# Optimization experiments

Hardware: AMD Instinct MI355X
Metric: run time of the kernel (lower is better)

The kernel has to match this reference:

```python
import jax, jax.numpy as jnp
import numpy as np

D_MODEL = 256
N_LEVELS = 4
N_HEADS = 8
N_POINTS = 4
OFF_DIM = 32
D_HEAD = D_MODEL // N_HEADS
SHAPES = [(64, 64), (32, 32), (16, 16), (8, 8)]  # (H_l, W_l)
LEN_IN = sum(h * w for h, w in SHAPES)  # 5440
N_BATCH = 4
LEN_Q = LEN_IN


def _offset_bias_init():
    # replicates _reset_parameters grid_init for sampling_offsets_bias
    thetas = np.arange(N_HEADS, dtype=np.float32) * (2.0 * np.pi / N_HEADS)
    grid = np.stack([np.cos(thetas), np.sin(thetas)], -1)
    grid = grid / np.abs(grid).max(-1, keepdims=True)
    grid = np.tile(grid[:, None, None, :], (1, N_LEVELS, N_POINTS, 1))
    grid = grid * np.arange(1, N_POINTS + 1, dtype=np.float32)[None, None, :, None]
    return jnp.asarray(grid, jnp.float32)  # (H, L, K, 2)


def setup_inputs() -> dict:
    key = jax.random.key(0)
    ks = jax.random.split(key, 12)
    s = 0.02
    return {
        "query": jax.random.normal(ks[0], (N_BATCH, LEN_Q, D_MODEL), jnp.float32),
        "reference_points": jax.random.uniform(ks[1], (N_BATCH, LEN_Q, N_LEVELS, 2), jnp.float32),
        "input_flatten": jax.random.normal(ks[2], (N_BATCH, LEN_IN, D_MODEL), jnp.float32),
        "input_spatial_shapes": jnp.asarray(SHAPES, jnp.int32),
        "offset_embeds_W": jax.random.normal(ks[3], (N_HEADS * N_LEVELS * N_POINTS * OFF_DIM, D_MODEL), jnp.float32) * s,
        "sampling_offsets_W": jax.random.normal(ks[4], (N_HEADS, N_LEVELS, N_POINTS, OFF_DIM, 2), jnp.float32) * s,
        "sampling_offsets_b": _offset_bias_init(),
        "attn_W": jax.random.normal(ks[5], (N_HEADS, N_LEVELS, N_POINTS, OFF_DIM, 1), jnp.float32) * s,
        "attn_b": jax.random.normal(ks[6], (N_HEADS, N_LEVELS, N_POINTS), jnp.float32) * s,
        "value_W": jax.random.normal(ks[7], (D_MODEL, D_MODEL), jnp.float32) * (1.0 / np.sqrt(D_MODEL)),
        "value_b": jnp.zeros((D_MODEL,), jnp.float32),
        "out_W": jax.random.normal(ks[8], (D_MODEL, D_MODEL), jnp.float32) * (1.0 / np.sqrt(D_MODEL)),
        "out_b": jnp.zeros((D_MODEL,), jnp.float32),
    }


def _bilinear(v, loc, H, W):
    # v: (N, heads, H*W, d_head); loc: (N, Lq, heads, K, 2) in [0,1] (x=width, y=height)
    # matches torch grid_sample(mode=bilinear, padding=zeros, align_corners=False)
    N, Lq, Hh, K, _ = loc.shape
    x = loc[..., 0] * W - 0.5
    y = loc[..., 1] * H - 0.5
    x0 = jnp.floor(x)
    y0 = jnp.floor(y)
    wx = (x - x0).transpose(0, 2, 1, 3).reshape(N, Hh, Lq * K)[..., None]
    wy = (y - y0).transpose(0, 2, 1, 3).reshape(N, Hh, Lq * K)[..., None]
    x0i = x0.astype(jnp.int32)
    y0i = y0.astype(jnp.int32)

    def gather(xi, yi):
        valid = (xi >= 0) & (xi < W) & (yi >= 0) & (yi < H)
        idx = jnp.clip(yi, 0, H - 1) * W + jnp.clip(xi, 0, W - 1)
        idx = idx.transpose(0, 2, 1, 3).reshape(N, Hh, Lq * K)
        g = jnp.take_along_axis(v, idx[..., None], axis=2)  # (N, heads, Lq*K, d)
        m = valid.transpose(0, 2, 1, 3).reshape(N, Hh, Lq * K)
        return g * m[..., None].astype(v.dtype)

    g00 = gather(x0i, y0i)
    g01 = gather(x0i + 1, y0i)
    g10 = gather(x0i, y0i + 1)
    g11 = gather(x0i + 1, y0i + 1)
    out = (g00 * (1 - wx) * (1 - wy) + g01 * wx * (1 - wy)
           + g10 * (1 - wx) * wy + g11 * wx * wy)
    return out.reshape(N, Hh, Lq, K, -1)  # (N, heads, Lq, K, d_head)


def _forward(query, reference_points, input_flatten,
             offset_embeds_W, sampling_offsets_W, sampling_offsets_b,
             attn_W, attn_b, value_W, value_b, out_W, out_b):
    N, Lq, _ = query.shape
    # value projection
    value = input_flatten @ value_W.T + value_b                      # (N, Lin, C)
    value = value.reshape(N, -1, N_HEADS, D_HEAD)                    # (N, Lin, H, d)

    # offset embedding + activation (offset_act_name == 'silu')
    oe = jax.nn.silu(query @ offset_embeds_W.T)                      # (N, Lq, H*L*K*off)
    oe = oe.reshape(N, Lq, N_HEADS, N_LEVELS, N_POINTS, OFF_DIM)

    offs = jnp.einsum('bqhlkd,hlkdc->bqhlkc', oe, sampling_offsets_W) + sampling_offsets_b
    aw = jnp.einsum('bqhlkd,hlkd->bqhlk', oe, attn_W[..., 0]) + attn_b
    aw = jax.nn.softmax(aw.reshape(N, Lq, N_HEADS, N_LEVELS * N_POINTS), axis=-1)
    aw = aw.reshape(N, Lq, N_HEADS, N_LEVELS, N_POINTS)

    # normalize offsets by (W_l, H_l) and add reference points (2-dim branch)
    normalizer = jnp.asarray([[w, h] for h, w in SHAPES], jnp.float32)  # (L, 2)
    loc = reference_points[:, :, None, :, None, :] + offs / normalizer[None, None, None, :, None, :]

    out = jnp.zeros((N, Lq, N_HEADS, D_HEAD), jnp.float32)
    start = 0
    for lvl, (H, W) in enumerate(SHAPES):
        v_l = value[:, start:start + H * W].transpose(0, 2, 1, 3)    # (N, heads, HW, d)
        sampled = _bilinear(v_l, loc[:, :, :, lvl], H, W)            # (N, heads, Lq, K, d)
        out = out + jnp.einsum('bhqkd,bqhk->bqhd', sampled, aw[:, :, :, lvl])
        start += H * W
    out = out.reshape(N, Lq, D_MODEL)
    return out @ out_W.T + out_b


def reference(query, reference_points, input_flatten, input_spatial_shapes,
              offset_embeds_W, sampling_offsets_W, sampling_offsets_b,
              attn_W, attn_b, value_W, value_b, out_W, out_b):
    # input_spatial_shapes matches SHAPES (static pyramid)
    return _forward(query, reference_points, input_flatten,
                    offset_embeds_W, sampling_offsets_W, sampling_offsets_b,
                    attn_W, attn_b, value_W, value_b, out_W, out_b)
```

## Files before the change

### kernel.cpp

```cpp
#include <hip/hip_runtime.h>
#include <hip/hip_bf16.h>

#define NB 4
#define LQ 5440
#define DM 256
#define NH 8
#define NL 4
#define NP 4
#define OFFD 32
#define DH 32
#define MTOT (NB * LQ)
#define OEN (NH * NL * NP * OFFD)
#define NGRP (NH * NL * NP)

typedef __attribute__((ext_vector_type(8))) short bf16x8;
typedef __attribute__((ext_vector_type(4))) float f32x4;
typedef unsigned int u32;

#define GLOAD_LDS16(gp, lp) \
    __builtin_amdgcn_global_load_lds((const __attribute__((address_space(1))) u32*)(gp), \
                                     (__attribute__((address_space(3))) u32*)(lp), 16, 0, 0)

__device__ __forceinline__ float bf2f(unsigned short u) {
    union { unsigned int i; float f; } v; v.i = ((unsigned int)u) << 16; return v.f;
}
__device__ __forceinline__ unsigned short f2bf(float x) {
    u32 u = __float_as_uint(x);
    u = u + 0x7fffu + ((u >> 16) & 1u);
    return (unsigned short)(u >> 16);
}
__device__ __forceinline__ u32 pk2(float a, float b) {
    u32 ua = __float_as_uint(a), ub = __float_as_uint(b);
    ua = ua + 0x7fffu + ((ua >> 16) & 1u);
    ub = ub + 0x7fffu + ((ub >> 16) & 1u);
    return (ua >> 16) | (ub & 0xffff0000u);
}
__device__ __forceinline__ float silu(float x) {
    float e = __expf(-x);
    return x * __builtin_amdgcn_rcpf(1.0f + e);
}

__global__ __launch_bounds__(256) void k_cvt2(
    const float* __restrict__ A, unsigned short* __restrict__ Ao,
    const float* __restrict__ B, unsigned short* __restrict__ Bo, int n4)
{
    int i = blockIdx.x * 256 + threadIdx.x;
    if (i >= n4) return;
    const float* src = blockIdx.y ? B : A;
    unsigned short* dst = blockIdx.y ? Bo : Ao;
    float4 v = *(const float4*)(src + (size_t)i * 4);
    ushort4 o;
    o.x = f2bf(v.x); o.y = f2bf(v.y); o.z = f2bf(v.z); o.w = f2bf(v.w);
    *(ushort4*)(dst + (size_t)i * 4) = o;
}
__global__ __launch_bounds__(256) void k_cvt3(
    const float* __restrict__ A, unsigned short* __restrict__ Ao, int nA4,
    const float* __restrict__ B, unsigned short* __restrict__ Bo, int nB4,
    const float* __restrict__ C, unsigned short* __restrict__ Co, int nC4,
    const float* __restrict__ SW, const float* __restrict__ AW,
    unsigned short* __restrict__ Rb)
{
    int i = blockIdx.x * 256 + threadIdx.x;
    if (blockIdx.y == 3) {
        if (i < 65536) {
            int gg = i >> 9, jo = (i >> 5) & 15, d = i & 31;
            float v = 0.f;
            if (jo == 0)      v = SW[(gg * 32 + d) * 2 + 0];
            else if (jo == 1) v = SW[(gg * 32 + d) * 2 + 1];
            else if (jo == 2) v = AW[gg * 32 + d];
            Rb[i] = f2bf(v);
        }
        return;
    }
    const float* src; unsigned short* dst; int n4;
    if (blockIdx.y == 0)      { src = A; dst = Ao; n4 = nA4; }
    else if (blockIdx.y == 1) { src = B; dst = Bo; n4 = nB4; }
    else                      { src = C; dst = Co; n4 = nC4; }
    if (i >= n4) return;
    float4 v = *(const float4*)(src + (size_t)i * 4);
    ushort4 o;
    o.x = f2bf(v.x); o.y = f2bf(v.y); o.z = f2bf(v.z); o.w = f2bf(v.w);
    *(ushort4*)(dst + (size_t)i * 4) = o;
}


__global__ __launch_bounds__(256) void k_oe_mfma(
    const unsigned short* __restrict__ Qb,
    const unsigned short* __restrict__ Wb,
    const unsigned short* __restrict__ Rb,
    const float* __restrict__ SB,
    const float* __restrict__ AB,
    float* __restrict__ offs_out,
    float* __restrict__ aw_out)
{
    __shared__ short sA[128 * 64];
    __shared__ short sB[128 * 64];
    int tid = threadIdx.x;
    int n0 = blockIdx.x * 128;
    int m0 = blockIdx.y * 128;

    int lane = tid & 63;
    int w = tid >> 6;
    int wA = w >> 1;
    int wB = w & 1;
    int lcol = lane & 15, quad = lane >> 4;

    int srow = tid >> 3;
    int sq = (tid & 7) ^ (srow & 7);
    const short* gA = (const short*)Qb + (size_t)(m0 + srow) * 256 + sq * 8;
    const short* gB = (const short*)Wb + (size_t)(n0 + srow) * 256 + sq * 8;
    short* lA = sA + w * 512;
    short* lB = sB + w * 512;

    f32x4 acc[4][4] = {};

    const short* pq = sA + (wB * 64 + lcol) * 64;
    const short* pw = sB + (wA * 64 + lcol) * 64;
    int rx7 = lcol & 7;
    int qa0 = (quad ^ rx7) * 8;
    int qa1 = ((4 + quad) ^ rx7) * 8;

    for (int kc = 0; kc < 256; kc += 64) {
#pragma unroll
        for (int j = 0; j < 4; j++) {
            GLOAD_LDS16(gA + kc + j * 32 * 256, lA + j * 2048);
            GLOAD_LDS16(gB + kc + j * 32 * 256, lB + j * 2048);
        }
        __syncthreads();
        bf16x8 a[4][2], b[4][2];
#pragma unroll
        for (int i = 0; i < 4; i++) {
            a[i][0] = *(const bf16x8*)(pw + i * 16 * 64 + qa0);
            a[i][1] = *(const bf16x8*)(pw + i * 16 * 64 + qa1);
            b[i][0] = *(const bf16x8*)(pq + i * 16 * 64 + qa0);
            b[i][1] = *(const bf16x8*)(pq + i * 16 * 64 + qa1);
        }
#pragma unroll
        for (int kh = 0; kh < 2; kh++)
#pragma unroll
            for (int i = 0; i < 4; i++)
#pragma unroll
                for (int j = 0; j < 4; j++)
                    acc[i][j] = __builtin_amdgcn_mfma_f32_16x16x32_bf16(
                        a[i][kh], b[j][kh], acc[i][j], 0, 0, 0);
        __syncthreads();
    }

    u32 ps[4][4][2];
#pragma unroll
    for (int i = 0; i < 4; i++)
#pragma unroll
        for (int j = 0; j < 4; j++) {
            ps[i][j][0] = pk2(silu(acc[i][j][0]), silu(acc[i][j][1]));
            ps[i][j][1] = pk2(silu(acc[i][j][2]), silu(acc[i][j][3]));
        }

    int srcbase = (quad & 1) * 32 + lcol;
    bool hi = quad >= 2;
    f32x4 zero = {};
#pragma unroll
    for (int g = 0; g < 2; g++) {
        int gg = (n0 + wA * 64 + g * 32) >> 5;
        bf16x8 afrag = *(const bf16x8*)(Rb + ((size_t)(gg * 16 + lcol) * 32 + quad * 8));
        float sb0 = SB[gg * 2 + 0], sb1 = SB[gg * 2 + 1], ab = AB[gg];
#pragma unroll
        for (int j = 0; j < 4; j++) {
            union { u32 u[4]; bf16x8 v; } bf;
#pragma unroll
            for (int b = 0; b < 2; b++) {
                int s = srcbase + b * 16;
#pragma unroll
                for (int c = 0; c < 2; c++) {
                    u32 x0 = (u32)__shfl((int)ps[2 * g + 0][j][c], s);
                    u32 x1 = (u32)__shfl((int)ps[2 * g + 1][j][c], s);
                    bf.u[b * 2 + c] = hi ? x1 : x0;
                }
            }
            f32x4 d2 = __builtin_amdgcn_mfma_f32_16x16x32_bf16(afrag, bf.v, zero, 0, 0, 0);
            if (quad == 0) {
                int m = m0 + wB * 64 + j * 16 + lcol;
                size_t oi = ((size_t)m * NGRP + gg) * 2;
                offs_out[oi + 0] = d2[0] + sb0;
                offs_out[oi + 1] = d2[1] + sb1;
                aw_out[(size_t)m * NGRP + gg] = d2[2] + ab;
            }
        }
    }
}

__global__ __launch_bounds__(256) void k_value_mfma(
    const unsigned short* __restrict__ Xb,
    const unsigned short* __restrict__ Wvb,
    const float* __restrict__ bias,
    unsigned short* __restrict__ Vtb)
{
    __shared__ short sA[128 * 64];
    __shared__ short sB[128 * 64];
    int tid = threadIdx.x;
    int n0 = blockIdx.x * 128;
    int m0 = blockIdx.y * 128;
    int lane = tid & 63;
    int w = tid >> 6;
    int wA = w >> 1;
    int wB = w & 1;
    int lcol = lane & 15, quad = lane >> 4;

    int srow = tid >> 3;
    int sq = (tid & 7) ^ (srow & 7);
    const short* gA = (const short*)Xb + (size_t)(m0 + srow) * 256 + sq * 8;
    const short* gB = (const short*)Wvb + (size_t)(n0 + srow) * 256 + sq * 8;
    short* lA = sA + w * 512;
    short* lB = sB + w * 512;

    f32x4 acc[4][4] = {};
    const short* px = sA + (wB * 64 + lcol) * 64;
    const short* pw = sB + (wA * 64 + lcol) * 64;
    int rx7 = lcol & 7;
    int qa0 = (quad ^ rx7) * 8;
    int qa1 = ((4 + quad) ^ rx7) * 8;

    for (int kc = 0; kc < 256; kc += 64) {
#pragma unroll
        for (int j = 0; j < 4; j++) {
            GLOAD_LDS16(gA + kc + j * 32 * 256, lA + j * 2048);
            GLOAD_LDS16(gB + kc + j * 32 * 256, lB + j * 2048);
        }
        __syncthreads();
        bf16x8 a[4][2], b[4][2];
#pragma unroll
        for (int i = 0; i < 4; i++) {
            a[i][0] = *(const bf16x8*)(pw + i * 16 * 64 + qa0);
            a[i][1] = *(const bf16x8*)(pw + i * 16 * 64 + qa1);
            b[i][0] = *(const bf16x8*)(px + i * 16 * 64 + qa0);
            b[i][1] = *(const bf16x8*)(px + i * 16 * 64 + qa1);
        }
#pragma unroll
        for (int kh = 0; kh < 2; kh++)
#pragma unroll
            for (int i = 0; i < 4; i++)
#pragma unroll
                for (int j = 0; j < 4; j++)
                    acc[i][j] = __builtin_amdgcn_mfma_f32_16x16x32_bf16(
                        a[i][kh], b[j][kh], acc[i][j], 0, 0, 0);
        __syncthreads();
    }

#pragma unroll
    for (int i = 0; i < 4; i++) {
        int nb4 = n0 + wA * 64 + i * 16 + quad * 4;
        int h = nb4 >> 5, db = nb4 & 31;
        float4 b4 = *(const float4*)&bias[nb4];
#pragma unroll
        for (int j = 0; j < 4; j++) {
            int m = m0 + wB * 64 + j * 16 + lcol;
            int b = m / LQ, q = m - b * LQ;
            u32 lo = pk2(acc[i][j][0] + b4.x, acc[i][j][1] + b4.y);
            u32 hi2 = pk2(acc[i][j][2] + b4.z, acc[i][j][3] + b4.w);
            char* dst = (char*)Vtb + ((((size_t)b * NH + h) * LQ + q) * DH + db) * 2;
            *(uint2*)dst = make_uint2(lo, hi2);
        }
    }
}

__global__ __launch_bounds__(256) void k_out_mfma(
    const unsigned short* __restrict__ Xb,
    const unsigned short* __restrict__ Wob,
    const float* __restrict__ bias,
    float* __restrict__ Out)
{
    __shared__ short sA[128 * 64];
    __shared__ short sB[128 * 64];
    int tid = threadIdx.x;
    int n0 = blockIdx.x * 128;
    int m0 = blockIdx.y * 128;
    int lane = tid & 63;
    int w = tid >> 6;
    int wm = w >> 1, wn = w & 1;
    int lcol = lane & 15, lrow = lane >> 4;

    int srow = tid >> 3;
    int sq = (tid & 7) ^ (srow & 7);
    const short* gA = (const short*)Xb + (size_t)(m0 + srow) * 256 + sq * 8;
    const short* gB = (const short*)Wob + (size_t)(n0 + srow) * 256 + sq * 8;
    short* lA = sA + w * 512;
    short* lB = sB + w * 512;

    f32x4 acc[4][4] = {};
    const short* pa = sA + (wm * 64 + lcol) * 64;
    const short* pb = sB + (wn * 64 + lcol) * 64;
    int rx7 = lcol & 7;
    int qa0 = (lrow ^ rx7) * 8;
    int qa1 = ((4 + lrow) ^ rx7) * 8;

    for (int kc = 0; kc < 256; kc += 64) {
#pragma unroll
        for (int j = 0; j < 4; j++) {
            GLOAD_LDS16(gA + kc + j * 32 * 256, lA + j * 2048);
            GLOAD_LDS16(gB + kc + j * 32 * 256, lB + j * 2048);
        }
        __syncthreads();
        bf16x8 a[4][2], b[4][2];
#pragma unroll
        for (int i = 0; i < 4; i++) {
            a[i][0] = *(const bf16x8*)(pa + i * 16 * 64 + qa0);
            a[i][1] = *(const bf16x8*)(pa + i * 16 * 64 + qa1);
            b[i][0] = *(const bf16x8*)(pb + i * 16 * 64 + qa0);
            b[i][1] = *(const bf16x8*)(pb + i * 16 * 64 + qa1);
        }
#pragma unroll
        for (int kh = 0; kh < 2; kh++)
#pragma unroll
            for (int mi = 0; mi < 4; mi++)
#pragma unroll
                for (int ni = 0; ni < 4; ni++)
                    acc[mi][ni] = __builtin_amdgcn_mfma_f32_16x16x32_bf16(
                        a[mi][kh], b[ni][kh], acc[mi][ni], 0, 0, 0);
        __syncthreads();
    }

#pragma unroll
    for (int mi = 0; mi < 4; mi++) {
#pragma unroll
        for (int ni = 0; ni < 4; ni++) {
            int n = n0 + wn * 64 + ni * 16 + lcol;
            float bn = bias[n];
#pragma unroll
            for (int r = 0; r < 4; r++) {
                int m = m0 + wm * 64 + mi * 16 + lrow * 4 + r;
                Out[(size_t)m * 256 + n] = acc[mi][ni][r] + bn;
            }
        }
    }
}

__global__ __launch_bounds__(256) void k_sample(
    const unsigned short* __restrict__ Vtb,
    const float* __restrict__ refp,
    const float* __restrict__ offs,
    const float* __restrict__ awl,
    unsigned short* __restrict__ atnb)
{
    int tid = threadIdx.x;
    int h = blockIdx.y;
    int m_base = blockIdx.x * 64;
    __shared__ int2 s_iw[64][65];

    {
        int q = tid >> 2, lev = tid & 3;
        int m = m_base + q;
        float4 aw4 = *(const float4*)&awl[(size_t)m * 128 + h * 16 + lev * 4];
        float4 of0 = *(const float4*)&offs[((size_t)m * 128 + h * 16 + lev * 4) * 2];
        float4 of1 = *(const float4*)&offs[((size_t)m * 128 + h * 16 + lev * 4) * 2 + 4];
        float rx = refp[(size_t)m * 8 + lev * 2 + 0];
        float ry = refp[(size_t)m * 8 + lev * 2 + 1];

        float lg[4] = {aw4.x, aw4.y, aw4.z, aw4.w};
        float mx = fmaxf(fmaxf(lg[0], lg[1]), fmaxf(lg[2], lg[3]));
        mx = fmaxf(mx, __shfl_xor(mx, 1));
        mx = fmaxf(mx, __shfl_xor(mx, 2));
        float e[4]; float s = 0.f;
#pragma unroll
        for (int k = 0; k < 4; k++) { e[k] = __expf(lg[k] - mx); s += e[k]; }
        s += __shfl_xor(s, 1);
        s += __shfl_xor(s, 2);
        float inv = __builtin_amdgcn_rcpf(s);

        int Wl = 64 >> lev;
        int base = (lev == 0) ? 0 : (lev == 1) ? 4096 : (lev == 2) ? 5120 : 5376;
        float fW = (float)Wl;
        float oxs[4] = {of0.x, of0.z, of1.x, of1.z};
        float oys[4] = {of0.y, of0.w, of1.y, of1.w};
#pragma unroll
        for (int k = 0; k < 4; k++) {
            float prob = e[k] * inv;
            float x = rx * fW + oxs[k] - 0.5f;
            float y = ry * fW + oys[k] - 0.5f;
            float x0f = floorf(x), y0f = floorf(y);
            float wx = x - x0f, wy = y - y0f;
            int x0 = (int)x0f, y0 = (int)y0f;
            int xc0 = min(max(x0, 0), Wl - 1), xc1 = min(max(x0 + 1, 0), Wl - 1);
            int yc0 = min(max(y0, 0), Wl - 1), yc1 = min(max(y0 + 1, 0), Wl - 1);
            float vx0 = (x0 >= 0 && x0 < Wl) ? 1.f : 0.f;
            float vx1 = (x0 + 1 >= 0 && x0 + 1 < Wl) ? 1.f : 0.f;
            float vy0 = (y0 >= 0 && y0 < Wl) ? 1.f : 0.f;
            float vy1 = (y0 + 1 >= 0 && y0 + 1 < Wl) ? 1.f : 0.f;
            int pi = (lev * 4 + k) * 4;
            s_iw[q][pi + 0] = make_int2((base + yc0 * Wl + xc0) * 64,
                                        __float_as_int(prob * (1.f - wx) * (1.f - wy) * vx0 * vy0));
            s_iw[q][pi + 1] = make_int2((base + yc0 * Wl + xc1) * 64,
                                        __float_as_int(prob * wx * (1.f - wy) * vx1 * vy0));
            s_iw[q][pi + 2] = make_int2((base + yc1 * Wl + xc0) * 64,
                                        __float_as_int(prob * (1.f - wx) * wy * vx0 * vy1));
            s_iw[q][pi + 3] = make_int2((base + yc1 * Wl + xc1) * 64,
                                        __float_as_int(prob * wx * wy * vx1 * vy1));
        }
    }
    __syncthreads();

    int b = m_base / LQ;
    const char* plane = (const char*)(Vtb + ((size_t)b * NH + h) * LQ * DH);
    for (int t = 0; t < 2; t++) {
        int task = tid + t * 256;
        int q = task >> 3, seg = task & 7;
        int m = m_base + q;
        const char* ph = plane + seg * 8;
        float a0 = 0.f, a1 = 0.f, a2 = 0.f, a3 = 0.f;
#pragma unroll 4
        for (int p = 0; p < 16; p++) {
#pragma unroll
            for (int c = 0; c < 4; c++) {
                int2 iw = s_iw[q][p * 4 + c];
                uint2 v = *(const uint2*)(ph + iw.x);
                float wgt = __int_as_float(iw.y);
                a0 += wgt * __uint_as_float(v.x << 16);
                a1 += wgt * __uint_as_float(v.x & 0xffff0000u);
                a2 += wgt * __uint_as_float(v.y << 16);
                a3 += wgt * __uint_as_float(v.y & 0xffff0000u);
            }
        }
        ((uint2*)atnb)[(size_t)m * 64 + h * 8 + seg] =
            make_uint2(pk2(a0, a1), pk2(a2, a3));
    }
}

extern "C" void kernel_launch(void* const* d_in, const int* in_sizes, int n_in,
                              void* d_out, int out_size, void* d_ws, size_t ws_size,
                              hipStream_t stream) {
    const float* query  = (const float*)d_in[0];
    const float* refp   = (const float*)d_in[1];
    const float* inflat = (const float*)d_in[2];
    const float* We  = (const float*)d_in[4];
    const float* SW  = (const float*)d_in[5];
    const float* SB  = (const float*)d_in[6];
    const float* AWw = (const float*)d_in[7];
    const float* ABb = (const float*)d_in[8];
    const float* VW  = (const float*)d_in[9];
    const float* Vb  = (const float*)d_in[10];
    const float* OW  = (const float*)d_in[11];
    const float* Ob  = (const float*)d_in[12];
    float* out = (float*)d_out;

    float* ws = (float*)d_ws;
    unsigned short* Vtb  = (unsigned short*)ws;
    float* offs          = ws + 2785280;
    float* awl           = offs + 5570560;
    unsigned short* Qbf  = (unsigned short*)(awl + 2785280);
    unsigned short* Webf = Qbf + 5570560;
    unsigned short* Xbf  = Webf + 1048576;
    unsigned short* Wvbf = Xbf + 5570560;
    unsigned short* OWbf = Wvbf + 65536;
    unsigned short* Rbf  = OWbf + 65536;
    unsigned short* atnb = Xbf;

    k_cvt2<<<dim3(5440, 2), 256, 0, stream>>>(query, Qbf, inflat, Xbf, MTOT * 256 / 4);
    k_cvt3<<<dim3(1024, 4), 256, 0, stream>>>(We, Webf, OEN * 256 / 4,
                                              VW, Wvbf, 256 * 256 / 4,
                                              OW, OWbf, 256 * 256 / 4,
                                              SW, AWw, Rbf);

    k_value_mfma<<<dim3(2, MTOT / 128), 256, 0, stream>>>(Xbf, Wvbf, Vb, Vtb);

    k_oe_mfma<<<dim3(OEN / 128, MTOT / 128), 256, 0, stream>>>(
        Qbf, Webf, Rbf, SB, ABb, offs, awl);

    k_sample<<<dim3(MTOT / 64, NH), 256, 0, stream>>>(Vtb, refp, offs, awl, atnb);

    k_out_mfma<<<dim3(2, MTOT / 128), 256, 0, stream>>>(atnb, OWbf, Ob, out);
}
```

Measured before the change: 245.2 us.

## Merge conversion kernels and fuse value GEMM into offset-embed GEMM launch

Merges the two fp32-to-bf16 conversion kernels into one launch and folds the value projection GEMM into the offset-embedding GEMM kernel as extra blocks in a flat 1-D grid. This removes launch overhead and lets the small value GEMM fill idle slots beside the large one. The sampling kernel is remapped to a 1-D grid with head as the fastest index, and each thread now gathers 16-byte vectors over 8 channels for one query instead of two passes of 8-byte loads. This trades fewer, wider gathers for less parallelism per query. The fused kernel also carries dead shared-memory writes and unused shared arrays.

Result: no change. 242.2 us (-1.3%).

```diff
diff --git a/kernel.cpp b/kernel.cpp
--- a/kernel.cpp
+++ b/kernel.cpp
@@ -40,64 +40,97 @@
     return x * __builtin_amdgcn_rcpf(1.0f + e);
 }
 
-__global__ __launch_bounds__(256) void k_cvt2(
-    const float* __restrict__ A, unsigned short* __restrict__ Ao,
-    const float* __restrict__ B, unsigned short* __restrict__ Bo, int n4)
-{
-    int i = blockIdx.x * 256 + threadIdx.x;
-    if (i >= n4) return;
-    const float* src = blockIdx.y ? B : A;
-    unsigned short* dst = blockIdx.y ? Bo : Ao;
-    float4 v = *(const float4*)(src + (size_t)i * 4);
-    ushort4 o;
-    o.x = f2bf(v.x); o.y = f2bf(v.y); o.z = f2bf(v.z); o.w = f2bf(v.w);
-    *(ushort4*)(dst + (size_t)i * 4) = o;
-}
-__global__ __launch_bounds__(256) void k_cvt3(
-    const float* __restrict__ A, unsigned short* __restrict__ Ao, int nA4,
-    const float* __restrict__ B, unsigned short* __restrict__ Bo, int nB4,
-    const float* __restrict__ C, unsigned short* __restrict__ Co, int nC4,
+__global__ __launch_bounds__(256) void k_cvt(
+    const float* __restrict__ Q,  unsigned short* __restrict__ Qo,
+    const float* __restrict__ X,  unsigned short* __restrict__ Xo,
+    const float* __restrict__ We, unsigned short* __restrict__ Weo,
+    const float* __restrict__ Wv, unsigned short* __restrict__ Wvo,
+    const float* __restrict__ OW, unsigned short* __restrict__ OWo,
     const float* __restrict__ SW, const float* __restrict__ AW,
     unsigned short* __restrict__ Rb)
 {
-    int i = blockIdx.x * 256 + threadIdx.x;
-    if (blockIdx.y == 3) {
-        if (i < 65536) {
-            int gg = i >> 9, jo = (i >> 5) & 15, d = i & 31;
-            float v = 0.f;
-            if (jo == 0)      v = SW[(gg * 32 + d) * 2 + 0];
-            else if (jo == 1) v = SW[(gg * 32 + d) * 2 + 1];
-            else if (jo == 2) v = AW[gg * 32 + d];
-            Rb[i] = f2bf(v);
-        }
+    int tid = threadIdx.x, x = blockIdx.x, y = blockIdx.y;
+    if (y < 2) {
+        const float* src = y ? X : Q;
+        unsigned short* dst = y ? Xo : Qo;
+        int i = x * 256 + tid;
+        float4 v = *(const float4*)(src + (size_t)i * 4);
+        ushort4 o;
+        o.x = f2bf(v.x); o.y = f2bf(v.y); o.z = f2bf(v.z); o.w = f2bf(v.w);
+        *(ushort4*)(dst + (size_t)i * 4) = o;
         return;
     }
-    const float* src; unsigned short* dst; int n4;
-    if (blockIdx.y == 0)      { src = A; dst = Ao; n4 = nA4; }
-    else if (blockIdx.y == 1) { src = B; dst = Bo; n4 = nB4; }
-    else                      { src = C; dst = Co; n4 = nC4; }
-    if (i >= n4) return;
-    float4 v = *(const float4*)(src + (size_t)i * 4);
-    ushort4 o;
-    o.x = f2bf(v.x); o.y = f2bf(v.y); o.z = f2bf(v.z); o.w = f2bf(v.w);
-    *(ushort4*)(dst + (size_t)i * 4) = o;
-}
-
-
-__global__ __launch_bounds__(256) void k_oe_mfma(
+    if (x < 1024) {
+        int i = x * 256 + tid;
+        float4 v = *(const float4*)(We + (size_t)i * 4);
+        ushort4 o;
+        o.x = f2bf(v.x); o.y = f2bf(v.y); o.z = f2bf(v.z); o.w = f2bf(v.w);
+        *(ushort4*)(Weo + (size_t)i * 4) = o;
+    } else if (x < 1088) {
+        int i = (x - 1024) * 256 + tid;
+        float4 v = *(const float4*)(Wv + (size_t)i * 4);
+        ushort4 o;
+        o.x = f2bf(v.x); o.y = f2bf(v.y); o.z = f2bf(v.z); o.w = f2bf(v.w);
+        *(ushort4*)(Wvo + (size_t)i * 4) = o;
+    } else if (x < 1152) {
+        int i = (x - 1088) * 256 + tid;
+        float4 v = *(const float4*)(OW + (size_t)i * 4);
+        ushort4 o;
+        o.x = f2bf(v.x); o.y = f2bf(v.y); o.z = f2bf(v.z); o.w = f2bf(v.w);
+        *(ushort4*)(OWo + (size_t)i * 4) = o;
+    } else if (x < 1408) {
+        int i = (x - 1152) * 256 + tid;
+        int gg = i >> 9, jo = (i >> 5) & 15, d = i & 31;
+        float v = 0.f;
+        if (jo == 0)      v = SW[(gg * 32 + d) * 2 + 0];
+        else if (jo == 1) v = SW[(gg * 32 + d) * 2 + 1];
+        else if (jo == 2) v = AW[gg * 32 + d];
+        Rb[i] = f2bf(v);
+    }
+}
+
+__global__ __launch_bounds__(256) void k_oeval_mfma(
     const unsigned short* __restrict__ Qb,
     const unsigned short* __restrict__ Wb,
+    const unsigned short* __restrict__ Xb,
+    const unsigned short* __restrict__ Wvb,
     const unsigned short* __restrict__ Rb,
     const float* __restrict__ SB,
     const float* __restrict__ AB,
+    const float* __restrict__ Vbias,
     float* __restrict__ offs_out,
-    float* __restrict__ aw_out)
+    float* __restrict__ aw_out,
+    unsigned short* __restrict__ Vtb)
 {
     __shared__ short sA[128 * 64];
     __shared__ short sB[128 * 64];
+    __shared__ float w0s[128], w1s[128], wAs[128];
+
     int tid = threadIdx.x;
-    int n0 = blockIdx.x * 128;
-    int m0 = blockIdx.y * 128;
+    int id = blockIdx.x;
+    bool is_oe = id < 5440;
+    int n0, m0;
+    const unsigned short *Ag, *Bg;
+    if (is_oe) {
+        n0 = (id & 31) * 128;
+        m0 = (id >> 5) * 128;
+        Ag = Qb; Bg = Wb;
+    } else {
+        int v = id - 5440;
+        n0 = (v & 1) * 128;
+        m0 = (v >> 1) * 128;
+        Ag = Xb; Bg = Wvb;
+    }
+
+    if (is_oe && tid < 128) {
+        int n = n0 + tid;
+        w0s[tid] = __ldg(&((const float*)SB)[0]) * 0.f + 0.f;
+    }
+    if (is_oe && tid < 128) {
+        int n = n0 + tid;
+        const float* SWx = (const float*)nullptr;
+        (void)SWx;
+    }
 
     int lane = tid & 63;
     int w = tid >> 6;
@@ -107,8 +140,8 @@
 
     int srow = tid >> 3;
     int sq = (tid & 7) ^ (srow & 7);
-    const short* gA = (const short*)Qb + (size_t)(m0 + srow) * 256 + sq * 8;
-    const short* gB = (const short*)Wb + (size_t)(n0 + srow) * 256 + sq * 8;
+    const short* gA = (const short*)Ag + (size_t)(m0 + srow) * 256 + sq * 8;
+    const short* gB = (const short*)Bg + (size_t)(n0 + srow) * 256 + sq * 8;
     short* lA = sA + w * 512;
     short* lB = sB + w * 512;
 
@@ -146,118 +179,62 @@
         __syncthreads();
     }
 
-    u32 ps[4][4][2];
-#pragma unroll
-    for (int i = 0; i < 4; i++)
-#pragma unroll
-        for (int j = 0; j < 4; j++) {
-            ps[i][j][0] = pk2(silu(acc[i][j][0]), silu(acc[i][j][1]));
-            ps[i][j][1] = pk2(silu(acc[i][j][2]), silu(acc[i][j][3]));
-        }
-
-    int srcbase = (quad & 1) * 32 + lcol;
-    bool hi = quad >= 2;
-    f32x4 zero = {};
-#pragma unroll
-    for (int g = 0; g < 2; g++) {
-        int gg = (n0 + wA * 64 + g * 32) >> 5;
-        bf16x8 afrag = *(const bf16x8*)(Rb + ((size_t)(gg * 16 + lcol) * 32 + quad * 8));
-        float sb0 = SB[gg * 2 + 0], sb1 = SB[gg * 2 + 1], ab = AB[gg];
-#pragma unroll
-        for (int j = 0; j < 4; j++) {
-            union { u32 u[4]; bf16x8 v; } bf;
-#pragma unroll
-            for (int b = 0; b < 2; b++) {
-                int s = srcbase + b * 16;
-#pragma unroll
-                for (int c = 0; c < 2; c++) {
-                    u32 x0 = (u32)__shfl((int)ps[2 * g + 0][j][c], s);
-                    u32 x1 = (u32)__shfl((int)ps[2 * g + 1][j][c], s);
-                    bf.u[b * 2 + c] = hi ? x1 : x0;
+    if (is_oe) {
+        u32 ps[4][4][2];
+#pragma unroll
+        for (int i = 0; i < 4; i++)
+#pragma unroll
+            for (int j = 0; j < 4; j++) {
+                ps[i][j][0] = pk2(silu(acc[i][j][0]), silu(acc[i][j][1]));
+                ps[i][j][1] = pk2(silu(acc[i][j][2]), silu(acc[i][j][3]));
+            }
+
+        int srcbase = (quad & 1) * 32 + lcol;
+        bool hi = quad >= 2;
+        f32x4 zero = {};
+#pragma unroll
+        for (int g = 0; g < 2; g++) {
+            int gg = (n0 + wA * 64 + g * 32) >> 5;
+            bf16x8 afrag = *(const bf16x8*)(Rb + ((size_t)(gg * 16 + lcol) * 32 + quad * 8));
+            float sb0 = SB[gg * 2 + 0], sb1 = SB[gg * 2 + 1], ab = AB[gg];
+#pragma unroll
+            for (int j = 0; j < 4; j++) {
+                union { u32 u[4]; bf16x8 v; } bf;
+#pragma unroll
+                for (int b = 0; b < 2; b++) {
+                    int s = srcbase + b * 16;
+#pragma unroll
+                    for (int c = 0; c < 2; c++) {
+                        u32 x0 = (u32)__shfl((int)ps[2 * g + 0][j][c], s);
+                        u32 x1 = (u32)__shfl((int)ps[2 * g + 1][j][c], s);
+                        bf.u[b * 2 + c] = hi ? x1 : x0;
+                    }
+                }
+                f32x4 d2 = __builtin_amdgcn_mfma_f32_16x16x32_bf16(afrag, bf.v, zero, 0, 0, 0);
+                if (quad == 0) {
+                    int m = m0 + wB * 64 + j * 16 + lcol;
+                    size_t oi = ((size_t)m * NGRP + gg) * 2;
+                    offs_out[oi + 0] = d2[0] + sb0;
+                    offs_out[oi + 1] = d2[1] + sb1;
+                    aw_out[(size_t)m * NGRP + gg] = d2[2] + ab;
                 }
             }
-            f32x4 d2 = __builtin_amdgcn_mfma_f32_16x16x32_bf16(afrag, bf.v, zero, 0, 0, 0);
-            if (quad == 0) {
+        }
+    } else {
+#pragma unroll
+        for (int i = 0; i < 4; i++) {
+            int nb4 = n0 + wA * 64 + i * 16 + quad * 4;
+            int h = nb4 >> 5, db = nb4 & 31;
+            float4 b4 = *(const float4*)&Vbias[nb4];
+#pragma unroll
+            for (int j = 0; j < 4; j++) {
                 int m = m0 + wB * 64 + j * 16 + lcol;
-                size_t oi = ((size_t)m * NGRP + gg) * 2;
-                offs_out[oi + 0] = d2[0] + sb0;
-                offs_out[oi + 1] = d2[1] + sb1;
-                aw_out[(size_t)m * NGRP + gg] = d2[2] + ab;
+                int b = m / LQ, q = m - b * LQ;
+                u32 lo = pk2(acc[i][j][0] + b4.x, acc[i][j][1] + b4.y);
+                u32 hi2 = pk2(acc[i][j][2] + b4.z, acc[i][j][3] + b4.w);
+                char* dst = (char*)Vtb + ((((size_t)b * NH + h) * LQ + q) * DH + db) * 2;
+                *(uint2*)dst = make_uint2(lo, hi2);
             }
-        }
-    }
-}
-
-__global__ __launch_bounds__(256) void k_value_mfma(
-    const unsigned short* __restrict__ Xb,
-    const unsigned short* __restrict__ Wvb,
-    const float* __restrict__ bias,
-    unsigned short* __restrict__ Vtb)
-{
-    __shared__ short sA[128 * 64];
-    __shared__ short sB[128 * 64];
-    int tid = threadIdx.x;
-    int n0 = blockIdx.x * 128;
-    int m0 = blockIdx.y * 128;
-    int lane = tid & 63;
-    int w = tid >> 6;
-    int wA = w >> 1;
-    int wB = w & 1;
-    int lcol = lane & 15, quad = lane >> 4;
-
-    int srow = tid >> 3;
-    int sq = (tid & 7) ^ (srow & 7);
-    const short* gA = (const short*)Xb + (size_t)(m0 + srow) * 256 + sq * 8;
-    const short* gB = (const short*)Wvb + (size_t)(n0 + srow) * 256 + sq * 8;
-    short* lA = sA + w * 512;
-    short* lB = sB + w * 512;
-
-    f32x4 acc[4][4] = {};
-    const short* px = sA + (wB * 64 + lcol) * 64;
-    const short* pw = sB + (wA * 64 + lcol) * 64;
-    int rx7 = lcol & 7;
-    int qa0 = (quad ^ rx7) * 8;
-    int qa1 = ((4 + quad) ^ rx7) * 8;
-
-    for (int kc = 0; kc < 256; kc += 64) {
-#pragma unroll
-        for (int j = 0; j < 4; j++) {
-            GLOAD_LDS16(gA + kc + j * 32 * 256, lA + j * 2048);
-            GLOAD_LDS16(gB + kc + j * 32 * 256, lB + j * 2048);
-        }
-        __syncthreads();
-        bf16x8 a[4][2], b[4][2];
-#pragma unroll
-        for (int i = 0; i < 4; i++) {
-            a[i][0] = *(const bf16x8*)(pw + i * 16 * 64 + qa0);
-            a[i][1] = *(const bf16x8*)(pw + i * 16 * 64 + qa1);
-            b[i][0] = *(const bf16x8*)(px + i * 16 * 64 + qa0);
-            b[i][1] = *(const bf16x8*)(px + i * 16 * 64 + qa1);
-        }
-#pragma unroll
-        for (int kh = 0; kh < 2; kh++)
-#pragma unroll
-            for (int i = 0; i < 4; i++)
-#pragma unroll
-                for (int j = 0; j < 4; j++)
-                    acc[i][j] = __builtin_amdgcn_mfma_f32_16x16x32_bf16(
-                        a[i][kh], b[j][kh], acc[i][j], 0, 0, 0);
-        __syncthreads();
-    }
-
-#pragma unroll
-    for (int i = 0; i < 4; i++) {
-        int nb4 = n0 + wA * 64 + i * 16 + quad * 4;
-        int h = nb4 >> 5, db = nb4 & 31;
-        float4 b4 = *(const float4*)&bias[nb4];
-#pragma unroll
-        for (int j = 0; j < 4; j++) {
-            int m = m0 + wB * 64 + j * 16 + lcol;
-            int b = m / LQ, q = m - b * LQ;
-            u32 lo = pk2(acc[i][j][0] + b4.x, acc[i][j][1] + b4.y);
-            u32 hi2 = pk2(acc[i][j][2] + b4.z, acc[i][j][3] + b4.w);
-            char* dst = (char*)Vtb + ((((size_t)b * NH + h) * LQ + q) * DH + db) * 2;
-            *(uint2*)dst = make_uint2(lo, hi2);
         }
     }
 }
@@ -341,8 +318,9 @@
     unsigned short* __restrict__ atnb)
 {
     int tid = threadIdx.x;
-    int h = blockIdx.y;
-    int m_base = blockIdx.x * 64;
+    int id = blockIdx.x;
+    int h = id & 7;
+    int m_base = (id >> 3) * 64;
     __shared__ int2 s_iw[64][65];
 
     {
@@ -397,30 +375,31 @@
     }
     __syncthreads();
 
-    int b = m_base / LQ;
-    const char* plane = (const char*)(Vtb + ((size_t)b * NH + h) * LQ * DH);
-    for (int t = 0; t < 2; t++) {
-        int task = tid + t * 256;
-        int q = task >> 3, seg = task & 7;
-        int m = m_base + q;
-        const char* ph = plane + seg * 8;
-        float a0 = 0.f, a1 = 0.f, a2 = 0.f, a3 = 0.f;
-#pragma unroll 4
-        for (int p = 0; p < 16; p++) {
-#pragma unroll
-            for (int c = 0; c < 4; c++) {
-                int2 iw = s_iw[q][p * 4 + c];
-                uint2 v = *(const uint2*)(ph + iw.x);
-                float wgt = __int_as_float(iw.y);
-                a0 += wgt * __uint_as_float(v.x << 16);
-                a1 += wgt * __uint_as_float(v.x & 0xffff0000u);
-                a2 += wgt * __uint_as_float(v.y << 16);
-                a3 += wgt * __uint_as_float(v.y & 0xffff0000u);
-            }
-        }
-        ((uint2*)atnb)[(size_t)m * 64 + h * 8 + seg] =
-            make_uint2(pk2(a0, a1), pk2(a2, a3));
-    }
+    int q = tid >> 2, seg = tid & 3;
+    int m = m_base + q;
+    int b = m / LQ;
+    const char* ph = (const char*)(Vtb + ((size_t)b * NH + h) * LQ * DH) + seg * 16;
+    float a0 = 0.f, a1 = 0.f, a2 = 0.f, a3 = 0.f;
+    float a4 = 0.f, a5 = 0.f, a6 = 0.f, a7 = 0.f;
+#pragma unroll 2
+    for (int p = 0; p < 16; p++) {
+#pragma unroll
+        for (int c = 0; c < 4; c++) {
+            int2 iw = s_iw[q][p * 4 + c];
+            uint4 v = *(const uint4*)(ph + iw.x);
+            float wgt = __int_as_float(iw.y);
+            a0 += wgt * __uint_as_float(v.x << 16);
+            a1 += wgt * __uint_as_float(v.x & 0xffff0000u);
+            a2 += wgt * __uint_as_float(v.y << 16);
+            a3 += wgt * __uint_as_float(v.y & 0xffff0000u);
+            a4 += wgt * __uint_as_float(v.z << 16);
+            a5 += wgt * __uint_as_float(v.z & 0xffff0000u);
+            a6 += wgt * __uint_as_float(v.w << 16);
+            a7 += wgt * __uint_as_float(v.w & 0xffff0000u);
+        }
+    }
+    ((uint4*)atnb)[(size_t)m * 32 + h * 4 + seg] =
+        make_uint4(pk2(a0, a1), pk2(a2, a3), pk2(a4, a5), pk2(a6, a7));
 }
 
 extern "C" void kernel_launch(void* const* d_in, const int* in_sizes, int n_in,
@@ -452,18 +431,14 @@
     unsigned short* Rbf  = OWbf + 65536;
     unsigned short* atnb = Xbf;
 
-    k_cvt2<<<dim3(5440, 2), 256, 0, stream>>>(query, Qbf, inflat, Xbf, MTOT * 256 / 4);
-    k_cvt3<<<dim3(1024, 4), 256, 0, stream>>>(We, Webf, OEN * 256 / 4,
-                                              VW, Wvbf, 256 * 256 / 4,
-                                              OW, OWbf, 256 * 256 / 4,
-                                              SW, AWw, Rbf);
-
-    k_value_mfma<<<dim3(2, MTOT / 128), 256, 0, stream>>>(Xbf, Wvbf, Vb, Vtb);
-
-    k_oe_mfma<<<dim3(OEN / 128, MTOT / 128), 256, 0, stream>>>(
-        Qbf, Webf, Rbf, SB, ABb, offs, awl);
-
-    k_sample<<<dim3(MTOT / 64, NH), 256, 0, stream>>>(Vtb, refp, offs, awl, atnb);
+    k_cvt<<<dim3(5440, 3), 256, 0, stream>>>(query, Qbf, inflat, Xbf,
+                                             We, Webf, VW, Wvbf, OW, OWbf,
+                                             SW, AWw, Rbf);
+
+    k_oeval_mfma<<<dim3(5780), 256, 0, stream>>>(
+        Qbf, Webf, Xbf, Wvbf, Rbf, SB, ABb, Vb, offs, awl, Vtb);
+
+    k_sample<<<dim3(2720), 256, 0, stream>>>(Vtb, refp, offs, awl, atnb);
 
     k_out_mfma<<<dim3(2, MTOT / 128), 256, 0, stream>>>(atnb, OWbf, Ob, out);
 }
```
